# Optimization experiments

Measured on AMD Instinct MI355X. Metric: run time of the kernel, lower is better.

Reference implementation:

```python
import jax, jax.numpy as jnp
import numpy as np

N = 100000      # nodes
E = 3200000     # edges (before self loops)
F_IN = 5        # node_features
SH = 32         # spatial_hidden
H = 8           # heads
C = SH // H     # per-head dim = 4
TH = 64         # temporal_hidden
TC = TH // 3    # 21 (trend/seasonal lstm hidden)
TR = TH - 2 * TC  # 22 (residual mlp)
SEQ = 14
CV_THRESH = 1.5


def setup_inputs() -> dict:
    key = jax.random.key(0)
    cnt = [0]
    def nk():
        cnt[0] += 1
        return jax.random.fold_in(key, cnt[0])
    def nrm(shape, s=0.1):
        return jax.random.normal(nk(), shape, jnp.float32) * s
    inp = {}
    inp['x'] = nrm((N, F_IN), 1.0)
    inp['edge_index'] = jax.random.randint(nk(), (2, E), 0, N)
    inp['trend'] = nrm((1, SEQ), 1.0)
    inp['seasonal'] = nrm((1, SEQ), 1.0)
    inp['residual'] = nrm((1, SEQ), 1.0)
    inp['cv_values'] = jax.random.uniform(nk(), (1,), jnp.float32, 0.0, 3.0)
    inp['target_store_idx'] = 42
    # GAT layers: layer0 in=F_IN, layers 1,2 in=SH
    for i, din in enumerate([F_IN, SH, SH]):
        inp[f'gat_W{i}'] = nrm((din, SH), 1.0 / np.sqrt(din))
        inp[f'gat_as{i}'] = nrm((H, C))
        inp[f'gat_ad{i}'] = nrm((H, C))
        inp[f'gat_b{i}'] = jnp.zeros((SH,), jnp.float32)
    # two 2-layer LSTMs (input sizes 1 then TC), PyTorch gate order i,f,g,o
    for p in ('t', 's'):
        for l, din in enumerate([1, TC]):
            inp[f'{p}_Wih{l}'] = nrm((4 * TC, din), 1.0 / np.sqrt(TC))
            inp[f'{p}_Whh{l}'] = nrm((4 * TC, TC), 1.0 / np.sqrt(TC))
            inp[f'{p}_bih{l}'] = jnp.zeros((4 * TC,), jnp.float32)
            inp[f'{p}_bhh{l}'] = jnp.zeros((4 * TC,), jnp.float32)
    inp['res_W'] = nrm((1, TR), 1.0)
    inp['res_b'] = jnp.zeros((TR,), jnp.float32)
    FU = SH + TH  # 96
    inp['pg_W'] = nrm((FU + 1, FU), 1.0 / np.sqrt(FU))
    inp['pg_b'] = jnp.zeros((FU,), jnp.float32)
    inp['f1_W'] = nrm((FU, TH), 1.0 / np.sqrt(FU))
    inp['f1_b'] = jnp.zeros((TH,), jnp.float32)
    inp['ln_g'] = jnp.ones((TH,), jnp.float32)
    inp['ln_b'] = jnp.zeros((TH,), jnp.float32)
    inp['f2_W'] = nrm((TH, TH // 2), 1.0 / np.sqrt(TH))
    inp['f2_b'] = jnp.zeros((TH // 2,), jnp.float32)
    inp['f3_W'] = nrm((TH // 2, SEQ), 1.0 / np.sqrt(TH // 2))
    inp['f3_b'] = jnp.zeros((SEQ,), jnp.float32)
    return inp


def _gat(h_in, src, dst, W, a_s, a_d, b):
    # PyG GATConv: message src->dst, softmax over incoming edges per dst
    h = (h_in @ W).reshape(-1, H, C)            # [N,H,C]
    es = jnp.einsum('nhc,hc->nh', h, a_s)       # [N,H]
    ed = jnp.einsum('nhc,hc->nh', h, a_d)
    e = jax.nn.leaky_relu(es[src] + ed[dst], 0.2)  # [Etot,H]
    emax = jax.ops.segment_max(e, dst, num_segments=N)
    emax = jnp.where(jnp.isfinite(emax), emax, 0.0)
    a = jnp.exp(e - emax[dst])
    den = jax.ops.segment_sum(a, dst, num_segments=N)
    a = a / (den[dst] + 1e-16)
    out = jax.ops.segment_sum(h[src] * a[..., None], dst, num_segments=N)
    return out.reshape(-1, H * C) + b


def _lstm2(x, params):
    # x: [B,T,in]; params: list of (Wih[4h,in], Whh[4h,h], bih, bhh)
    seq = x
    for (Wih, Whh, bih, bhh) in params:
        B = seq.shape[0]
        hh = Whh.shape[1]
        def step(carry, xt):
            hprev, cprev = carry
            g = xt @ Wih.T + hprev @ Whh.T + bih + bhh
            i, f, gg, o = jnp.split(g, 4, axis=-1)
            c = jax.nn.sigmoid(f) * cprev + jax.nn.sigmoid(i) * jnp.tanh(gg)
            hn = jax.nn.sigmoid(o) * jnp.tanh(c)
            return (hn, c), hn
        init = (jnp.zeros((B, hh), seq.dtype), jnp.zeros((B, hh), seq.dtype))
        _, ys = jax.lax.scan(step, init, jnp.swapaxes(seq, 0, 1))
        seq = jnp.swapaxes(ys, 0, 1)
    return seq


def _forward(x, trend, seasonal, residual, cv_values,
             gat_params, lstm_t, lstm_s,
             res_W, res_b, pg_W, pg_b,
             f1_W, f1_b, ln_g, ln_b, f2_W, f2_b, f3_W, f3_b,
             edge_index, target_store_idx):
    loops = jnp.arange(N, dtype=edge_index.dtype)  # add_self_loops=True
    src = jnp.concatenate([edge_index[0], loops])
    dst = jnp.concatenate([edge_index[1], loops])
    h = x
    for (W, a_s, a_d, b) in gat_params:
        h = jax.nn.elu(_gat(h, src, dst, W, a_s, a_d, b))
    target_spatial = h[target_store_idx][None, :]          # [1,SH]
    trend_out = _lstm2(trend[..., None], lstm_t)[:, -1, :]      # [1,TC]
    seasonal_out = _lstm2(seasonal[..., None], lstm_s)[:, -1, :]
    res_out = jax.nn.relu(residual[..., None] @ res_W + res_b)[:, -1, :]  # [1,TR]
    temporal = jnp.concatenate([trend_out, seasonal_out, res_out], -1)    # [1,TH]
    combined = jnp.concatenate([target_spatial, temporal], -1)            # [1,96]
    gated_in = jnp.concatenate([combined, cv_values[:, None]], -1)        # [1,97]
    gate = jax.nn.sigmoid(gated_in @ pg_W + pg_b)
    gf = combined * gate
    h1 = gf @ f1_W + f1_b
    mu = h1.mean(-1, keepdims=True)
    var = h1.var(-1, keepdims=True)
    h1 = jax.nn.relu((h1 - mu) / jnp.sqrt(var + 1e-5) * ln_g + ln_b)
    h2 = jax.nn.relu(h1 @ f2_W + f2_b)
    return h2 @ f3_W + f3_b                                 # [1,SEQ]


def reference(x, edge_index, trend, seasonal, residual, cv_values, target_store_idx,
              gat_W0, gat_as0, gat_ad0, gat_b0,
              gat_W1, gat_as1, gat_ad1, gat_b1,
              gat_W2, gat_as2, gat_ad2, gat_b2,
              t_Wih0, t_Whh0, t_bih0, t_bhh0, t_Wih1, t_Whh1, t_bih1, t_bhh1,
              s_Wih0, s_Whh0, s_bih0, s_bhh0, s_Wih1, s_Whh1, s_bih1, s_bhh1,
              res_W, res_b, pg_W, pg_b,
              f1_W, f1_b, ln_g, ln_b, f2_W, f2_b, f3_W, f3_b):
    gat_params = [(gat_W0, gat_as0, gat_ad0, gat_b0),
                  (gat_W1, gat_as1, gat_ad1, gat_b1),
                  (gat_W2, gat_as2, gat_ad2, gat_b2)]
    lstm_t = [(t_Wih0, t_Whh0, t_bih0, t_bhh0), (t_Wih1, t_Whh1, t_bih1, t_bhh1)]
    lstm_s = [(s_Wih0, s_Whh0, s_bih0, s_bhh0), (s_Wih1, s_Whh1, s_bih1, s_bhh1)]
    return _forward(x, trend, seasonal, residual, cv_values,
                    gat_params, lstm_t, lstm_s,
                    res_W, res_b, pg_W, pg_b,
                    f1_W, f1_b, ln_g, ln_b, f2_W, f2_b, f3_W, f3_b,
                    edge_index, target_store_idx)
```

## Files before the change

kernel.cpp:

```cpp
#include <hip/hip_runtime.h>
#include <hip/hip_bf16.h>
#include <stdint.h>
#include <math.h>

#define NN   100000
#define EE   3200000
#define FIN  5
#define SHD  32
#define NH   8
#define TCH  21
#define TRH  22
#define SEQL 14

#define ECA   1024
#define ECL1  1024
#define ECL2  8192
#define RSTR  96

#define BCHK2 4096
#define NBC2  ((EE + BCHK2 - 1) / BCHK2)
#define NBW   ((NN + 31) / 32)
#define NBWP  3200

typedef __hip_bfloat16 bf16;
typedef __attribute__((ext_vector_type(2))) float f32x2;

__device__ __forceinline__ float b2f(bf16 v) { return __bfloat162float(v); }
__device__ __forceinline__ float sigm(float x) { return 1.f / (1.f + __expf(-x)); }
__device__ __forceinline__ float ldw(const void* p, int i, int f) {
    return f ? ((const float*)p)[i] : __bfloat162float(((const bf16*)p)[i]);
}
__device__ __forceinline__ float relu_nan(float v) {
    return (v == v) ? ((v > 0.f) ? v : 0.f) : v;
}
__device__ __forceinline__ unsigned short f2b(float v) {
    bf16 b = __float2bfloat16(v);
    return *reinterpret_cast<unsigned short*>(&b);
}
__device__ __forceinline__ float cvf(float v) { return v; }
__device__ __forceinline__ float cvf(bf16 v) { return __bfloat162float(v); }
__device__ __forceinline__ void cp(float* dst, const void* src, int n,
                                   int t0, int stride, int f) {
    if (f) {
        const float* s = (const float*)src;
        for (int i = t0; i < n; i += stride) dst[i] = s[i];
    } else {
        const bf16* s = (const bf16*)src;
        for (int i = t0; i < n; i += stride) dst[i] = b2f(s[i]);
    }
}

__global__ void PatternAwareSTGAT_94489281309_kernel(const unsigned int* xw, int* flag,
        const void* as0, const void* b0, const void* as1, const void* b1,
        const void* as2, const void* b2, float* prm) {
    int tid = threadIdx.x;
    int sane = 0;
    for (int i = 0; i < 64; i++) {
        unsigned int lo = xw[i] & 0xFFFFu;
        int e = (int)((lo >> 7) & 0xFF);
        if (e >= 110 && e <= 135) sane++;
    }
    int f = (sane >= 32) ? 0 : 1;
    if (tid == 0) flag[0] = f;
    const void* asp[3] = {as0, as1, as2};
    const void* bp[3]  = {b0, b1, b2};
    for (int l = 0; l < 3; l++)
        prm[l * 64 + tid] = (tid < 32) ? ldw(asp[l], tid, f) : ldw(bp[l], tid - 32, f);
}

__global__ __launch_bounds__(256) void k_scanA(
        const int* __restrict__ ei, const int* __restrict__ tgtp,
        int* __restrict__ eA, int* __restrict__ cA,
        unsigned* __restrict__ bm1, int* __restrict__ l1, int* __restrict__ c1,
        unsigned* __restrict__ bm2, int* __restrict__ l2, int* __restrict__ c2,
        int* __restrict__ l3, int* __restrict__ c3) {
    int tid = threadIdx.x;
    int tgtv = tgtp[0];
    if (blockIdx.x == 0 && tid == 0) {
        unsigned bit = 1u << (tgtv & 31);
        unsigned old = atomicOr(&bm1[tgtv >> 5], bit);
        if (!(old & bit)) { int p = atomicAdd(c1, 1); if (p < ECL1) l1[p] = tgtv; }
        old = atomicOr(&bm2[tgtv >> 5], bit);
        if (!(old & bit)) { int p = atomicAdd(c2, 1); if (p < ECL2) l2[p] = tgtv; }
        l3[0] = tgtv; c3[0] = 1;
    }
    int e0 = blockIdx.x * BCHK2 + tid * 16;
    if (e0 >= EE) return;
    const int4* dd4 = (const int4*)(ei + EE + e0);
    int4 a = dd4[0], b = dd4[1], c = dd4[2], d = dd4[3];
    int dv[16];
    dv[0]=a.x; dv[1]=a.y; dv[2]=a.z; dv[3]=a.w;
    dv[4]=b.x; dv[5]=b.y; dv[6]=b.z; dv[7]=b.w;
    dv[8]=c.x; dv[9]=c.y; dv[10]=c.z; dv[11]=c.w;
    dv[12]=d.x; dv[13]=d.y; dv[14]=d.z; dv[15]=d.w;
    unsigned mask = 0;
#pragma unroll
    for (int j = 0; j < 16; j++) if (dv[j] == tgtv) mask |= (1u << j);
    if (!mask) return;
#pragma unroll
    for (int j = 0; j < 16; j++) {
        if (mask & (1u << j)) {
            int s = ei[e0 + j];
            int p = atomicAdd(cA, 1);
            if (p < ECA) eA[p] = s;
            unsigned bit = 1u << (s & 31);
            unsigned old = atomicOr(&bm1[s >> 5], bit);
            if (!(old & bit)) { int q = atomicAdd(c1, 1); if (q < ECL1) l1[q] = s; }
            old = atomicOr(&bm2[s >> 5], bit);
            if (!(old & bit)) { int q = atomicAdd(c2, 1); if (q < ECL2) l2[q] = s; }
        }
    }
}

__global__ __launch_bounds__(256) void k_scanR(
        const int* __restrict__ ei, const unsigned* __restrict__ bm,
        int* __restrict__ fill, int* __restrict__ rows,
        unsigned* __restrict__ bmN, int* __restrict__ lN,
        int* __restrict__ cN, int capN) {
    __shared__ unsigned sbm[NBWP];
    int tid = threadIdx.x;
    {
        const uint4* b4 = (const uint4*)bm;
        uint4* s4 = (uint4*)sbm;
        uint4 t0 = b4[tid];
        uint4 t1 = b4[tid + 256];
        uint4 t2 = (tid + 512 < NBWP / 4) ? b4[tid + 512] : make_uint4(0,0,0,0);
        uint4 t3 = (tid + 768 < NBWP / 4) ? b4[tid + 768] : make_uint4(0,0,0,0);
        s4[tid] = t0;
        s4[tid + 256] = t1;
        if (tid + 512 < NBWP / 4) s4[tid + 512] = t2;
        if (tid + 768 < NBWP / 4) s4[tid + 768] = t3;
    }
    __syncthreads();
    int e0 = blockIdx.x * BCHK2 + tid * 16;
    if (e0 >= EE) return;
    const int4* dd4 = (const int4*)(ei + EE + e0);
    int4 a = dd4[0], b = dd4[1], c = dd4[2], d = dd4[3];
    int dv[16];
    dv[0]=a.x; dv[1]=a.y; dv[2]=a.z; dv[3]=a.w;
    dv[4]=b.x; dv[5]=b.y; dv[6]=b.z; dv[7]=b.w;
    dv[8]=c.x; dv[9]=c.y; dv[10]=c.z; dv[11]=c.w;
    dv[12]=d.x; dv[13]=d.y; dv[14]=d.z; dv[15]=d.w;
    unsigned mask = 0;
#pragma unroll
    for (int j = 0; j < 16; j++)
        if ((sbm[dv[j] >> 5] >> (dv[j] & 31)) & 1u) mask |= (1u << j);
    if (!mask) return;
#pragma unroll
    for (int j = 0; j < 16; j++) {
        if (mask & (1u << j)) {
            int dn = dv[j];
            int s = ei[e0 + j];
            int p = atomicAdd(&fill[dn], 1);
            if (p < RSTR) rows[(size_t)dn * RSTR + p] = s;
            if (bmN) {
                unsigned bit = 1u << (s & 31);
                unsigned old = atomicOr(&bmN[s >> 5], bit);
                if (!(old & bit)) {
                    int q = atomicAdd(cN, 1);
                    if (q < capN) lN[q] = s;
                }
            }
        }
    }
}

__global__ void k_transform0(const void* x, const void* W, const void* ad_,
                             const int* flag, unsigned short* hWb, float* ed) {
    __shared__ float sW[FIN * SHD];
    __shared__ float sad[SHD];
    int tid = threadIdx.x;
    int f = flag[0];
    cp(sW, W, FIN * SHD, tid, 256, f);
    if (tid >= 192 && tid < 192 + SHD) sad[tid - 192] = ldw(ad_, tid - 192, f);
    __syncthreads();
    int n = blockIdx.x * 256 + tid;
    if (n >= NN) return;
    float xr[FIN];
    if (f) {
        const float* xp = (const float*)x + (size_t)n * FIN;
        for (int k = 0; k < FIN; k++) xr[k] = xp[k];
    } else {
        const bf16* xp = (const bf16*)x + (size_t)n * FIN;
        for (int k = 0; k < FIN; k++) xr[k] = b2f(xp[k]);
    }
    float o[SHD];
    for (int j = 0; j < SHD; j++) o[j] = 0.f;
    for (int k = 0; k < FIN; k++) {
        float xv = xr[k];
        for (int j = 0; j < SHD; j++) o[j] += xv * sW[k * SHD + j];
    }
    ushort4* row = (ushort4*)(hWb + (size_t)n * SHD);
    for (int q = 0; q < 8; q++) {
        ushort4 v; v.x = f2b(o[q*4]); v.y = f2b(o[q*4+1]); v.z = f2b(o[q*4+2]); v.w = f2b(o[q*4+3]);
        row[q] = v;
    }
    for (int h = 0; h < NH; h++) {
        float e2 = 0.f;
        for (int c = 0; c < 4; c++) e2 += o[h * 4 + c] * sad[h * 4 + c];
        ed[(size_t)n * NH + h] = e2;
    }
}

__global__ void k_transform1(const int* __restrict__ list, const int* __restrict__ cntp,
                             int cap,
                             const float* x, const void* W, const void* ad_,
                             const int* flag, unsigned short* hWb, float* ed) {
    __shared__ float sW[SHD * SHD];
    __shared__ float sad[SHD];
    int tid = threadIdx.x;
    int f = flag[0];
    cp(sW, W, SHD * SHD, tid, 256, f);
    if (tid >= 192 && tid < 192 + SHD) sad[tid - 192] = ldw(ad_, tid - 192, f);
    __syncthreads();
    int cnt = cntp[0]; if (cnt > cap) cnt = cap;
    int ii = blockIdx.x * 256 + tid;
    if (ii >= cnt) return;
    int n = list[ii];
    float xr[SHD];
    const float4* xp4 = (const float4*)(x + (size_t)n * SHD);
#pragma unroll
    for (int q = 0; q < 8; q++) {
        float4 v = xp4[q];
        xr[q*4] = v.x; xr[q*4+1] = v.y; xr[q*4+2] = v.z; xr[q*4+3] = v.w;
    }
    float o[SHD];
    for (int j = 0; j < SHD; j++) o[j] = 0.f;
    for (int k = 0; k < SHD; k++) {
        float xv = xr[k];
        for (int j = 0; j < SHD; j++) o[j] += xv * sW[k * SHD + j];
    }
    ushort4* row = (ushort4*)(hWb + (size_t)n * SHD);
    for (int q = 0; q < 8; q++) {
        ushort4 v; v.x = f2b(o[q*4]); v.y = f2b(o[q*4+1]); v.z = f2b(o[q*4+2]); v.w = f2b(o[q*4+3]);
        row[q] = v;
    }
    for (int h = 0; h < NH; h++) {
        float e2 = 0.f;
        for (int c = 0; c < 4; c++) e2 += o[h * 4 + c] * sad[h * 4 + c];
        ed[(size_t)n * NH + h] = e2;
    }
}

__global__ void k_aggregate(const int* __restrict__ list, const int* __restrict__ cntp,
                            int cap,
                            const int* __restrict__ rdeg,
                            const int* __restrict__ csr,
                            const int* __restrict__ ovr, int ovrCap,
                            const unsigned short* __restrict__ hWb,
                            const float* __restrict__ ed,
                            const float* __restrict__ prm,
                            float* __restrict__ out) {
    int gid = blockIdx.x * 256 + threadIdx.x;
    int lane = threadIdx.x & 63;
    int cnt = cntp[0]; if (cnt > cap) cnt = cap;
    int idx = (gid >> 6) * 2 + (lane >> 5);
    if (idx >= cnt) return;
    int n = list[idx];
    int l32 = lane & 31;
    int h = l32 & 7, k = l32 >> 3;
    float4 asv = *(const float4*)(prm + h * 4);
    float ednh = ed[(size_t)n * NH + h];
    int base, deg;
    if (ovr) { base = 0; deg = ovr[0]; if (deg > ovrCap) deg = ovrCap; }
    else     { base = n * RSTR; deg = rdeg[n]; if (deg > RSTR) deg = RSTR; }
    float den = 0.f;
    f32x2 acc01 = {0.f, 0.f}, acc23 = {0.f, 0.f};
    int t = k;
    int s0 = -1, s1 = -1, s2 = -1, s3 = -1, s4 = -1, s5 = -1;
    if (t <= deg)      s0 = (t == 0) ? n : __builtin_nontemporal_load(csr + base + t - 1);
    if (t + 4 <= deg)  s1 = __builtin_nontemporal_load(csr + base + t + 3);
    if (t + 8 <= deg)  s2 = __builtin_nontemporal_load(csr + base + t + 7);
    if (t + 12 <= deg) s3 = __builtin_nontemporal_load(csr + base + t + 11);
    if (t + 16 <= deg) s4 = __builtin_nontemporal_load(csr + base + t + 15);
    if (t + 20 <= deg) s5 = __builtin_nontemporal_load(csr + base + t + 19);
    while (s0 >= 0) {
        uint2 hv0 = *(const uint2*)(hWb + (size_t)s0 * SHD + h * 4);
        bool b1 = (s1 >= 0), b2 = (s2 >= 0), b3 = (s3 >= 0), b4 = (s4 >= 0), b5 = (s5 >= 0);
        uint2 hv1, hv2, hv3, hv4, hv5;
        if (b1) hv1 = *(const uint2*)(hWb + (size_t)s1 * SHD + h * 4);
        if (b2) hv2 = *(const uint2*)(hWb + (size_t)s2 * SHD + h * 4);
        if (b3) hv3 = *(const uint2*)(hWb + (size_t)s3 * SHD + h * 4);
        if (b4) hv4 = *(const uint2*)(hWb + (size_t)s4 * SHD + h * 4);
        if (b5) hv5 = *(const uint2*)(hWb + (size_t)s5 * SHD + h * 4);
        int tn = t + 24;
        int p0 = -1, p1 = -1, p2 = -1, p3 = -1, p4 = -1, p5 = -1;
        if (tn <= deg)      p0 = __builtin_nontemporal_load(csr + base + tn - 1);
        if (tn + 4 <= deg)  p1 = __builtin_nontemporal_load(csr + base + tn + 3);
        if (tn + 8 <= deg)  p2 = __builtin_nontemporal_load(csr + base + tn + 7);
        if (tn + 12 <= deg) p3 = __builtin_nontemporal_load(csr + base + tn + 11);
        if (tn + 16 <= deg) p4 = __builtin_nontemporal_load(csr + base + tn + 15);
        if (tn + 20 <= deg) p5 = __builtin_nontemporal_load(csr + base + tn + 19);
        {
            f32x2 h01, h23;
            h01.x = __uint_as_float(hv0.x << 16);
            h01.y = __uint_as_float(hv0.x & 0xffff0000u);
            h23.x = __uint_as_float(hv0.y << 16);
            h23.y = __uint_as_float(hv0.y & 0xffff0000u);
            f32x2 d2 = h01 * (f32x2){asv.x, asv.y} + h23 * (f32x2){asv.z, asv.w};
            float e = d2.x + d2.y + ednh;
            e = fmaxf(e, 0.2f * e);
            float a = __expf(e);
            den += a;
            f32x2 av = {a, a};
            acc01 += av * h01;
            acc23 += av * h23;
        }
        if (b1) {
            f32x2 h01, h23;
            h01.x = __uint_as_float(hv1.x << 16);
            h01.y = __uint_as_float(hv1.x & 0xffff0000u);
            h23.x = __uint_as_float(hv1.y << 16);
            h23.y = __uint_as_float(hv1.y & 0xffff0000u);
            f32x2 d2 = h01 * (f32x2){asv.x, asv.y} + h23 * (f32x2){asv.z, asv.w};
            float e = d2.x + d2.y + ednh;
            e = fmaxf(e, 0.2f * e);
            float a = __expf(e);
            den += a;
            f32x2 av = {a, a};
            acc01 += av * h01;
            acc23 += av * h23;
        }
        if (b2) {
            f32x2 h01, h23;
            h01.x = __uint_as_float(hv2.x << 16);
            h01.y = __uint_as_float(hv2.x & 0xffff0000u);
            h23.x = __uint_as_float(hv2.y << 16);
            h23.y = __uint_as_float(hv2.y & 0xffff0000u);
            f32x2 d2 = h01 * (f32x2){asv.x, asv.y} + h23 * (f32x2){asv.z, asv.w};
            float e = d2.x + d2.y + ednh;
            e = fmaxf(e, 0.2f * e);
            float a = __expf(e);
            den += a;
            f32x2 av = {a, a};
            acc01 += av * h01;
            acc23 += av * h23;
        }
        if (b3) {
            f32x2 h01, h23;
            h01.x = __uint_as_float(hv3.x << 16);
            h01.y = __uint_as_float(hv3.x & 0xffff0000u);
            h23.x = __uint_as_float(hv3.y << 16);
            h23.y = __uint_as_float(hv3.y & 0xffff0000u);
            f32x2 d2 = h01 * (f32x2){asv.x, asv.y} + h23 * (f32x2){asv.z, asv.w};
            float e = d2.x + d2.y + ednh;
            e = fmaxf(e, 0.2f * e);
            float a = __expf(e);
            den += a;
            f32x2 av = {a, a};
            acc01 += av * h01;
            acc23 += av * h23;
        }
        if (b4) {
            f32x2 h01, h23;
            h01.x = __uint_as_float(hv4.x << 16);
            h01.y = __uint_as_float(hv4.x & 0xffff0000u);
            h23.x = __uint_as_float(hv4.y << 16);
            h23.y = __uint_as_float(hv4.y & 0xffff0000u);
            f32x2 d2 = h01 * (f32x2){asv.x, asv.y} + h23 * (f32x2){asv.z, asv.w};
            float e = d2.x + d2.y + ednh;
            e = fmaxf(e, 0.2f * e);
            float a = __expf(e);
            den += a;
            f32x2 av = {a, a};
            acc01 += av * h01;
            acc23 += av * h23;
        }
        if (b5) {
            f32x2 h01, h23;
            h01.x = __uint_as_float(hv5.x << 16);
            h01.y = __uint_as_float(hv5.x & 0xffff0000u);
            h23.x = __uint_as_float(hv5.y << 16);
            h23.y = __uint_as_float(hv5.y & 0xffff0000u);
            f32x2 d2 = h01 * (f32x2){asv.x, asv.y} + h23 * (f32x2){asv.z, asv.w};
            float e = d2.x + d2.y + ednh;
            e = fmaxf(e, 0.2f * e);
            float a = __expf(e);
            den += a;
            f32x2 av = {a, a};
            acc01 += av * h01;
            acc23 += av * h23;
        }
        s0 = p0; s1 = p1; s2 = p2; s3 = p3; s4 = p4; s5 = p5; t = tn;
    }
    for (int off = 16; off >= 8; off >>= 1) {
        den      += __shfl_down(den, off, 32);
        acc01.x  += __shfl_down(acc01.x, off, 32);
        acc01.y  += __shfl_down(acc01.y, off, 32);
        acc23.x  += __shfl_down(acc23.x, off, 32);
        acc23.y  += __shfl_down(acc23.y, off, 32);
    }
    if (k == 0) {
        float inv = 1.f / (den + 1e-16f);
        float4 bv = *(const float4*)(prm + 32 + h * 4);
        float v0 = acc01.x * inv + bv.x;
        float v1 = acc01.y * inv + bv.y;
        float v2 = acc23.x * inv + bv.z;
        float v3 = acc23.y * inv + bv.w;
        v0 = (v0 > 0.f) ? v0 : expm1f(v0);
        v1 = (v1 > 0.f) ? v1 : expm1f(v1);
        v2 = (v2 > 0.f) ? v2 : expm1f(v2);
        v3 = (v3 > 0.f) ? v3 : expm1f(v3);
        *(float4*)(out + (size_t)n * SHD + h * 4) = make_float4(v0, v1, v2, v3);
    }
}

template<typename T>
__device__ __forceinline__ void lstm_load_regs(
        const T* Wih0, const T* Whh0, const T* bih0, const T* bhh0,
        const T* Wih1, const T* Whh1, const T* bih1, const T* bhh1,
        const T* xin, int l, bool bl, float* xs,
        float& wa, float& ba, float& wb, float& bb, float& ba2, float& bb2,
        float* Wa, float* Wb, float* Ua, float* Va, float* Ub, float* Vb) {
#pragma unroll
    for (int t = 0; t < SEQL; t++) xs[t] = cvf(xin[t]);
    wa = cvf(Wih0[l]);
    ba = cvf(bih0[l]) + cvf(bhh0[l]);
    wb = bl ? cvf(Wih0[64 + l]) : 0.f;
    bb = bl ? (cvf(bih0[64 + l]) + cvf(bhh0[64 + l])) : 0.f;
    ba2 = cvf(bih1[l]) + cvf(bhh1[l]);
    bb2 = bl ? (cvf(bih1[64 + l]) + cvf(bhh1[64 + l])) : 0.f;
#pragma unroll
    for (int j = 0; j < 21; j++) {
        Wa[j] = cvf(Whh0[l * 21 + j]);
        Wb[j] = bl ? cvf(Whh0[(64 + l) * 21 + j]) : 0.f;
        Ua[j] = cvf(Wih1[l * 21 + j]);
        Va[j] = cvf(Whh1[l * 21 + j]);
        Ub[j] = bl ? cvf(Wih1[(64 + l) * 21 + j]) : 0.f;
        Vb[j] = bl ? cvf(Whh1[(64 + l) * 21 + j]) : 0.f;
    }
}

__device__ __forceinline__ void warm_sweep(const void* p, int nbytes, int t2) {
    const uint4* s = (const uint4*)p;
    int nv = nbytes >> 4;
    unsigned acc = 0;
    for (int i = t2; i < nv; i += 1024) {
        uint4 v0 = s[i];
        uint4 v1 = (i + 128 < nv) ? s[i + 128] : make_uint4(0,0,0,0);
        uint4 v2 = (i + 256 < nv) ? s[i + 256] : make_uint4(0,0,0,0);
        uint4 v3 = (i + 384 < nv) ? s[i + 384] : make_uint4(0,0,0,0);
        uint4 v4 = (i + 512 < nv) ? s[i + 512] : make_uint4(0,0,0,0);
        uint4 v5 = (i + 640 < nv) ? s[i + 640] : make_uint4(0,0,0,0);
        uint4 v6 = (i + 768 < nv) ? s[i + 768] : make_uint4(0,0,0,0);
        uint4 v7 = (i + 896 < nv) ? s[i + 896] : make_uint4(0,0,0,0);
        acc ^= v0.x ^ v1.x ^ v2.x ^ v3.x ^ v4.x ^ v5.x ^ v6.x ^ v7.x;
    }
    asm volatile("" :: "v"(acc));
}

template<typename T>
__device__ __forceinline__ float matvec_t(const T* W, const float* vin,
                                          float bias, int n, int col, int ncol) {
    float acc = bias;
    int k2 = 0;
    for (; k2 + 8 <= n; k2 += 8) {
        float w0 = cvf(W[(k2 + 0) * ncol + col]);
        float w1 = cvf(W[(k2 + 1) * ncol + col]);
        float w2 = cvf(W[(k2 + 2) * ncol + col]);
        float w3 = cvf(W[(k2 + 3) * ncol + col]);
        float w4 = cvf(W[(k2 + 4) * ncol + col]);
        float w5 = cvf(W[(k2 + 5) * ncol + col]);
        float w6 = cvf(W[(k2 + 6) * ncol + col]);
        float w7 = cvf(W[(k2 + 7) * ncol + col]);
        acc += vin[k2 + 0] * w0; acc += vin[k2 + 1] * w1;
        acc += vin[k2 + 2] * w2; acc += vin[k2 + 3] * w3;
        acc += vin[k2 + 4] * w4; acc += vin[k2 + 5] * w5;
        acc += vin[k2 + 6] * w6; acc += vin[k2 + 7] * w7;
    }
    for (; k2 < n; k2++) acc += vin[k2] * cvf(W[k2 * ncol + col]);
    return acc;
}
__device__ __forceinline__ float matvec(const void* W, const float* vin,
                                        float bias, int n, int col, int ncol, int f) {
    return f ? matvec_t<float>((const float*)W, vin, bias, n, col, ncol)
             : matvec_t<bf16>((const bf16*)W, vin, bias, n, col, ncol);
}

__global__ __launch_bounds__(256, 1)
void k_tail(const void* trend, const void* seasonal, const void* residual,
                       const void* cv, const int* tgtp,
                       const void* tWih0, const void* tWhh0, const void* tbih0, const void* tbhh0,
                       const void* tWih1, const void* tWhh1, const void* tbih1, const void* tbhh1,
                       const void* sWih0, const void* sWhh0, const void* sbih0, const void* sbhh0,
                       const void* sWih1, const void* sWhh1, const void* sbih1, const void* sbhh1,
                       const void* res_W, const void* res_b,
                       const void* pg_W, const void* pg_b,
                       const void* f1_W, const void* f1_b,
                       const void* ln_g, const void* ln_b,
                       const void* f2_W, const void* f2_b,
                       const void* f3_W, const void* f3_b,
                       const int* flag, const float* A, void* out) {
    __shared__ __align__(16) float SH1[2][24];
    __shared__ __align__(16) float SH2[2][24];
    __shared__ float comb[97];
    __shared__ float gf[96];
    __shared__ float h1v[64];
    __shared__ float h2s[32];
    __shared__ float sbias[336];
    __shared__ float stats[2];
    const int tid = threadIdx.x;
    const int f = flag[0];
    const int w = tid >> 6, l = tid & 63;

    if (tid < 96) {
        if (tid < 48) SH1[tid / 24][tid % 24] = 0.f;
        else { int u = tid - 48; SH2[u / 24][u % 24] = 0.f; }
    }
    __syncthreads();

    if (w < 2) {
        const void* Wih0 = w ? sWih0 : tWih0;
        const void* Whh0 = w ? sWhh0 : tWhh0;
        const void* bih0 = w ? sbih0 : tbih0;
        const void* bhh0 = w ? sbhh0 : tbhh0;
        const void* Wih1 = w ? sWih1 : tWih1;
        const void* Whh1 = w ? sWhh1 : tWhh1;
        const void* bih1 = w ? sbih1 : tbih1;
        const void* bhh1 = w ? sbhh1 : tbhh1;
        const void* xin  = w ? seasonal : trend;
        const bool bl = (l < 20);
        float xs[SEQL];
        float wa, ba, wb, bb, ba2, bb2;
        float Wa[21], Wb[21], Ua[21], Va[21], Ub[21], Vb[21];
        if (f) {
            lstm_load_regs<float>((const float*)Wih0, (const float*)Whh0,
                (const float*)bih0, (const float*)bhh0,
                (const float*)Wih1, (const float*)Whh1,
                (const float*)bih1, (const float*)bhh1,
                (const float*)xin, l, bl, xs, wa, ba, wb, bb, ba2, bb2,
                Wa, Wb, Ua, Va, Ub, Vb);
        } else {
            lstm_load_regs<bf16>((const bf16*)Wih0, (const bf16*)Whh0,
                (const bf16*)bih0, (const bf16*)bhh0,
                (const bf16*)Wih1, (const bf16*)Whh1,
                (const bf16*)bih1, (const bf16*)bhh1,
                (const bf16*)xin, l, bl, xs, wa, ba, wb, bb, ba2, bb2,
                Wa, Wb, Ua, Va, Ub, Vb);
        }
#pragma unroll
        for (int j = 0; j < 21; j++) {
            asm volatile("" : "+v"(Wa[j]), "+v"(Wb[j]));
            asm volatile("" : "+v"(Ua[j]), "+v"(Va[j]));
            asm volatile("" : "+v"(Ub[j]), "+v"(Vb[j]));
        }
#pragma unroll
        for (int t = 0; t < SEQL; t++) asm volatile("" : "+v"(xs[t]));
        asm volatile("" : "+v"(wa), "+v"(ba));
        asm volatile("" : "+v"(wb), "+v"(bb));
        asm volatile("" : "+v"(ba2), "+v"(bb2));

        float h1r = 0.f, c1v = 0.f, h2r = 0.f, c2v = 0.f;
#pragma unroll 1
        for (int t = 0; t < SEQL; t++) {
            float aa = ba + xs[t] * wa;
            float ab = bb + xs[t] * wb;
#pragma unroll
            for (int q = 0; q < 5; q++) {
                float4 v = *(const float4*)&SH1[w][q * 4];
                aa += v.x * Wa[q*4];   ab += v.x * Wb[q*4];
                aa += v.y * Wa[q*4+1]; ab += v.y * Wb[q*4+1];
                aa += v.z * Wa[q*4+2]; ab += v.z * Wb[q*4+2];
                aa += v.w * Wa[q*4+3]; ab += v.w * Wb[q*4+3];
            }
            { float v20 = SH1[w][20]; aa += v20 * Wa[20]; ab += v20 * Wb[20]; }
            float fj = __shfl(aa, 21 + l);
            float gj = __shfl(aa, 42 + l);
            float oa = __shfl(aa, 63);
            float ob = __shfl(ab, (l == 0) ? 0 : (l - 1));
            float oj = (l == 0) ? oa : ob;
            if (l < 21) {
                c1v = sigm(fj) * c1v + sigm(aa) * tanhf(gj);
                h1r = sigm(oj) * tanhf(c1v);
                SH1[w][l] = h1r;
            }
            __threadfence_block();
            float a2 = ba2, b2v = bb2;
#pragma unroll
            for (int q = 0; q < 5; q++) {
                float4 u = *(const float4*)&SH1[w][q * 4];
                float4 v = *(const float4*)&SH2[w][q * 4];
                a2  += u.x * Ua[q*4]   + v.x * Va[q*4];
                b2v += u.x * Ub[q*4]   + v.x * Vb[q*4];
                a2  += u.y * Ua[q*4+1] + v.y * Va[q*4+1];
                b2v += u.y * Ub[q*4+1] + v.y * Vb[q*4+1];
                a2  += u.z * Ua[q*4+2] + v.z * Va[q*4+2];
                b2v += u.z * Ub[q*4+2] + v.z * Vb[q*4+2];
                a2  += u.w * Ua[q*4+3] + v.w * Va[q*4+3];
                b2v += u.w * Ub[q*4+3] + v.w * Vb[q*4+3];
            }
            { float u20 = SH1[w][20], v20 = SH2[w][20];
              a2  += u20 * Ua[20] + v20 * Va[20];
              b2v += u20 * Ub[20] + v20 * Vb[20]; }
            float fj2 = __shfl(a2, 21 + l);
            float gj2 = __shfl(a2, 42 + l);
            float oa2 = __shfl(a2, 63);
            float ob2 = __shfl(b2v, (l == 0) ? 0 : (l - 1));
            float oj2 = (l == 0) ? oa2 : ob2;
            if (l < 21) {
                c2v = sigm(fj2) * c2v + sigm(a2) * tanhf(gj2);
                h2r = sigm(oj2) * tanhf(c2v);
                SH2[w][l] = h2r;
            }
            __threadfence_block();
        }
        if (l < 21) comb[(w == 0 ? 32 : 53) + l] = h2r;
    } else {
        int t2 = tid - 128;
        if (t2 < TRH)
            comb[74 + t2] = relu_nan(ldw(residual, SEQL - 1, f) * ldw(res_W, t2, f)
                                     + ldw(res_b, t2, f));
        if (t2 == TRH) comb[96] = ldw(cv, 0, f);
        if (t2 >= 32 && t2 < 64) {
            int tgt = tgtp[0];
            comb[t2 - 32] = A[(size_t)tgt * SHD + (t2 - 32)];
        }
        for (int i = t2; i < 336; i += 128) {
            float v;
            if (i < 96)       v = ldw(pg_b, i, f);
            else if (i < 160) v = ldw(f1_b, i - 96, f);
            else if (i < 192) v = ldw(f2_b, i - 160, f);
            else if (i < 206) v = ldw(f3_b, i - 192, f);
            else if (i < 208) v = 0.f;
            else if (i < 272) v = ldw(ln_g, i - 208, f);
            else              v = ldw(ln_b, i - 272, f);
            sbias[i] = v;
        }
        int esz = f ? 4 : 2;
        warm_sweep(pg_W, 9312 * esz, t2);
        warm_sweep(f1_W, 6144 * esz, t2);
        warm_sweep(f2_W, 2048 * esz, t2);
        warm_sweep(f3_W,  448 * esz, t2);
    }
    __syncthreads();

    if (tid < 96)
        gf[tid] = comb[tid] * sigm(matvec(pg_W, comb, sbias[tid], 97, tid, 96, f));
    __syncthreads();
    if (tid < 64)
        h1v[tid] = matvec(f1_W, gf, sbias[96 + tid], 96, tid, 64, f);
    __syncthreads();
    if (tid == 0) {
        float mu = 0.f;
        for (int j = 0; j < 64; j++) mu += h1v[j];
        mu /= 64.f;
        float var = 0.f;
        for (int j = 0; j < 64; j++) { float d = h1v[j] - mu; var += d * d; }
        var /= 64.f;
        stats[0] = mu; stats[1] = rsqrtf(var + 1e-5f);
    }
    __syncthreads();
    if (tid < 64)
        h1v[tid] = relu_nan((h1v[tid] - stats[0]) * stats[1] * sbias[208 + tid] + sbias[272 + tid]);
    __syncthreads();
    if (tid < 32)
        h2s[tid] = relu_nan(matvec(f2_W, h1v, sbias[160 + tid], 64, tid, 32, f));
    __syncthreads();
    if (tid < SEQL) {
        float acc = matvec(f3_W, h2s, sbias[192 + tid], 32, tid, 14, f);
        if (acc != acc) acc = 3333.0f;
        if (f) ((float*)out)[tid] = acc;
        else   ((bf16*)out)[tid] = __float2bfloat16(acc);
    }
}

static inline unsigned short h_f2bf(float f) {
    union { float f; unsigned u; } x; x.f = f;
    return (unsigned short)(x.u >> 16);
}
static unsigned short g_diag[SEQL];

extern "C" void kernel_launch(void* const* d_in, const int* in_sizes, int n_in,
                              void* d_out, int out_size, void* d_ws, size_t ws_size,
                              hipStream_t stream) {
    const int* ei  = (const int*)d_in[1];
    const int* tgt = (const int*)d_in[6];

    const size_t HWB  = sizeof(unsigned short) * (size_t)NN * SHD;
    const size_t EDB  = sizeof(float) * (size_t)NN * NH;
    const size_t AB   = sizeof(float) * (size_t)NN * SHD;
    const size_t ZER  = sizeof(int) * (size_t)(16 + 2 * NBWP + 2 * NN);
    const size_t ROWB = sizeof(int) * (size_t)NN * RSTR;
    const size_t LSTB = sizeof(int) * (size_t)(ECA + ECL1 + 8 + ECL2);
    const size_t NEED = 256 + 1024 + ZER + LSTB + 2 * ROWB + 512 + HWB + EDB + AB;
    if (ws_size < NEED) {
        for (int i = 0; i < SEQL; i++) g_diag[i] = h_f2bf(7777.0f);
        hipMemcpyAsync(d_out, g_diag, SEQL * sizeof(unsigned short),
                       hipMemcpyHostToDevice, stream);
        return;
    }

    char* p = (char*)d_ws;
    int*   flag = (int*)p;   p += 256;
    float* prm  = (float*)p; p += 1024;
    int* cnts  = (int*)p; p += sizeof(int) * 16;
    unsigned* bm1 = (unsigned*)p; p += sizeof(int) * NBWP;
    unsigned* bm2 = (unsigned*)p; p += sizeof(int) * NBWP;
    int* fillB = (int*)p; p += sizeof(int) * NN;
    int* fillC = (int*)p; p += sizeof(int) * NN;
    int* eA   = (int*)p; p += sizeof(int) * ECA;
    int* l1   = (int*)p; p += sizeof(int) * ECL1;
    int* l3   = (int*)p; p += sizeof(int) * 8;
    int* l2   = (int*)p; p += sizeof(int) * ECL2;
    int* rowsB = (int*)p; p += ROWB;
    int* rowsC = (int*)p; p += ROWB;
    p = (char*)(((uintptr_t)p + 255) & ~(uintptr_t)255);
    unsigned short* hWb = (unsigned short*)p; p += HWB;
    float* ed = (float*)p; p += EDB;
    float* A  = (float*)p; p += AB;
    int* cA = cnts; int* c1 = cnts + 1; int* c2 = cnts + 2; int* c3 = cnts + 3;

    dim3 b256(256);
    dim3 gN((NN + 255) / 256);
    dim3 gScan(NBC2);

    PatternAwareSTGAT_94489281309_kernel<<<dim3(1), dim3(64), 0, stream>>>(
        (const unsigned int*)d_in[0], flag,
        d_in[8], d_in[10], d_in[12], d_in[14], d_in[16], d_in[18], prm);

    hipMemsetAsync(cnts, 0, ZER, stream);

    k_scanA<<<gScan, b256, 0, stream>>>(ei, tgt, eA, cA,
                                        bm1, l1, c1, bm2, l2, c2, l3, c3);
    k_scanR<<<gScan, b256, 0, stream>>>(ei, bm1, fillB, rowsB,
                                        bm2, l2, c2, ECL2);
    k_scanR<<<gScan, b256, 0, stream>>>(ei, bm2, fillC, rowsC,
                                        (unsigned*)nullptr, (int*)nullptr,
                                        (int*)nullptr, 0);

    k_transform0<<<gN, b256, 0, stream>>>(d_in[0], d_in[7], d_in[9], flag, hWb, ed);
    k_aggregate<<<dim3(ECL2 * 32 / 256), b256, 0, stream>>>(l2, c2, ECL2,
        fillC, rowsC, (const int*)nullptr, 0, hWb, ed, prm, A);
    k_transform1<<<dim3(ECL2 / 256), b256, 0, stream>>>(l2, c2, ECL2,
        A, d_in[11], d_in[13], flag, hWb, ed);
    k_aggregate<<<dim3(ECL1 * 32 / 256), b256, 0, stream>>>(l1, c1, ECL1,
        fillB, rowsB, (const int*)nullptr, 0, hWb, ed, prm + 64, A);
    k_transform1<<<dim3((ECL1 + 255) / 256), b256, 0, stream>>>(l1, c1, ECL1,
        A, d_in[15], d_in[17], flag, hWb, ed);
    k_aggregate<<<dim3(1), b256, 0, stream>>>(l3, c3, 8,
        (const int*)nullptr, eA, cA, ECA, hWb, ed, prm + 128, A);

    k_tail<<<dim3(1), b256, 0, stream>>>(
        d_in[2], d_in[3], d_in[4], d_in[5], tgt,
        d_in[19], d_in[20], d_in[21], d_in[22],
        d_in[23], d_in[24], d_in[25], d_in[26],
        d_in[27], d_in[28], d_in[29], d_in[30],
        d_in[31], d_in[32], d_in[33], d_in[34],
        d_in[35], d_in[36],
        d_in[37], d_in[38],
        d_in[39], d_in[40],
        d_in[41], d_in[42],
        d_in[43], d_in[44],
        d_in[45], d_in[46],
        flag, A, d_out);
}
```

Before: 255.6 us.

## Fuse final-layer target aggregation into tail kernel and drop separate edge list

The third GAT layer's aggregation for the single target node now runs inside the tail kernel, in one spare warp, reading the existing rowsB CSR rows instead of a dedicated eA edge list. This removes one kernel launch, the A round-trip for the target row, and the per-match atomics into eA and cA inside the scan. The sanity check in the setup kernel now uses a wavefront ballot instead of a serial 64-element loop. The tradeoff is that the fused aggregation runs in a single warp and sits on the tail kernel's critical path, and the target's degree is capped at RSTR where the old list allowed up to ECA.

```diff
diff --git a/kernel.cpp b/kernel.cpp
--- a/kernel.cpp
+++ b/kernel.cpp
@@ -12,7 +12,6 @@
 #define TRH  22
 #define SEQL 14
 
-#define ECA   1024
 #define ECL1  1024
 #define ECL2  8192
 #define RSTR  96
@@ -54,12 +53,10 @@
         const void* as0, const void* b0, const void* as1, const void* b1,
         const void* as2, const void* b2, float* prm) {
     int tid = threadIdx.x;
-    int sane = 0;
-    for (int i = 0; i < 64; i++) {
-        unsigned int lo = xw[i] & 0xFFFFu;
-        int e = (int)((lo >> 7) & 0xFF);
-        if (e >= 110 && e <= 135) sane++;
-    }
+    unsigned int lo = xw[tid] & 0xFFFFu;
+    int e = (int)((lo >> 7) & 0xFF);
+    bool ok = (e >= 110 && e <= 135);
+    int sane = __popcll(__ballot(ok));
     int f = (sane >= 32) ? 0 : 1;
     if (tid == 0) flag[0] = f;
     const void* asp[3] = {as0, as1, as2};
@@ -70,10 +67,8 @@
 
 __global__ __launch_bounds__(256) void k_scanA(
         const int* __restrict__ ei, const int* __restrict__ tgtp,
-        int* __restrict__ eA, int* __restrict__ cA,
         unsigned* __restrict__ bm1, int* __restrict__ l1, int* __restrict__ c1,
-        unsigned* __restrict__ bm2, int* __restrict__ l2, int* __restrict__ c2,
-        int* __restrict__ l3, int* __restrict__ c3) {
+        unsigned* __restrict__ bm2, int* __restrict__ l2, int* __restrict__ c2) {
     int tid = threadIdx.x;
     int tgtv = tgtp[0];
     if (blockIdx.x == 0 && tid == 0) {
@@ -82,7 +77,6 @@
         if (!(old & bit)) { int p = atomicAdd(c1, 1); if (p < ECL1) l1[p] = tgtv; }
         old = atomicOr(&bm2[tgtv >> 5], bit);
         if (!(old & bit)) { int p = atomicAdd(c2, 1); if (p < ECL2) l2[p] = tgtv; }
-        l3[0] = tgtv; c3[0] = 1;
     }
     int e0 = blockIdx.x * BCHK2 + tid * 16;
     if (e0 >= EE) return;
@@ -101,8 +95,6 @@
     for (int j = 0; j < 16; j++) {
         if (mask & (1u << j)) {
             int s = ei[e0 + j];
-            int p = atomicAdd(cA, 1);
-            if (p < ECA) eA[p] = s;
             unsigned bit = 1u << (s & 31);
             unsigned old = atomicOr(&bm1[s >> 5], bit);
             if (!(old & bit)) { int q = atomicAdd(c1, 1); if (q < ECL1) l1[q] = s; }
@@ -246,7 +238,6 @@
                             int cap,
                             const int* __restrict__ rdeg,
                             const int* __restrict__ csr,
-                            const int* __restrict__ ovr, int ovrCap,
                             const unsigned short* __restrict__ hWb,
                             const float* __restrict__ ed,
                             const float* __restrict__ prm,
@@ -261,9 +252,8 @@
     int h = l32 & 7, k = l32 >> 3;
     float4 asv = *(const float4*)(prm + h * 4);
     float ednh = ed[(size_t)n * NH + h];
-    int base, deg;
-    if (ovr) { base = 0; deg = ovr[0]; if (deg > ovrCap) deg = ovrCap; }
-    else     { base = n * RSTR; deg = rdeg[n]; if (deg > RSTR) deg = RSTR; }
+    int base = n * RSTR;
+    int deg = rdeg[n]; if (deg > RSTR) deg = RSTR;
     float den = 0.f;
     f32x2 acc01 = {0.f, 0.f}, acc23 = {0.f, 0.f};
     int t = k;
@@ -490,10 +480,15 @@
                        const void* ln_g, const void* ln_b,
                        const void* f2_W, const void* f2_b,
                        const void* f3_W, const void* f3_b,
-                       const int* flag, const float* A, void* out) {
+                       const int* flag,
+                       const int* __restrict__ rowsB, const int* __restrict__ fillB,
+                       const unsigned short* __restrict__ hWb,
+                       const float* __restrict__ ed,
+                       const float* __restrict__ prm3,
+                       void* out) {
     __shared__ __align__(16) float SH1[2][24];
     __shared__ __align__(16) float SH2[2][24];
-    __shared__ float comb[97];
+    __shared__ __align__(16) float comb[100];
     __shared__ float gf[96];
     __shared__ float h1v[64];
     __shared__ float h2s[32];
@@ -611,10 +606,6 @@
             comb[74 + t2] = relu_nan(ldw(residual, SEQL - 1, f) * ldw(res_W, t2, f)
                                      + ldw(res_b, t2, f));
         if (t2 == TRH) comb[96] = ldw(cv, 0, f);
-        if (t2 >= 32 && t2 < 64) {
-            int tgt = tgtp[0];
-            comb[t2 - 32] = A[(size_t)tgt * SHD + (t2 - 32)];
-        }
         for (int i = t2; i < 336; i += 128) {
             float v;
             if (i < 96)       v = ldw(pg_b, i, f);
@@ -631,6 +622,155 @@
         warm_sweep(f1_W, 6144 * esz, t2);
         warm_sweep(f2_W, 2048 * esz, t2);
         warm_sweep(f3_W,  448 * esz, t2);
+
+        if (w == 2 && l < 32) {
+            int tgt = tgtp[0];
+            int h = l & 7, k = l >> 3;
+            float4 asv = *(const float4*)(prm3 + h * 4);
+            float ednh = ed[(size_t)tgt * NH + h];
+            int base = tgt * RSTR;
+            int deg = fillB[tgt]; if (deg > RSTR) deg = RSTR;
+            float den = 0.f;
+            f32x2 acc01 = {0.f, 0.f}, acc23 = {0.f, 0.f};
+            int t = k;
+            int s0 = -1, s1 = -1, s2 = -1, s3 = -1, s4 = -1, s5 = -1;
+            if (t <= deg)      s0 = (t == 0) ? tgt : rowsB[base + t - 1];
+            if (t + 4 <= deg)  s1 = rowsB[base + t + 3];
+            if (t + 8 <= deg)  s2 = rowsB[base + t + 7];
+            if (t + 12 <= deg) s3 = rowsB[base + t + 11];
+            if (t + 16 <= deg) s4 = rowsB[base + t + 15];
+            if (t + 20 <= deg) s5 = rowsB[base + t + 19];
+            while (s0 >= 0) {
+                uint2 hv0 = *(const uint2*)(hWb + (size_t)s0 * SHD + h * 4);
+                bool b1 = (s1 >= 0), b2 = (s2 >= 0), b3 = (s3 >= 0),
+                     b4 = (s4 >= 0), b5 = (s5 >= 0);
+                uint2 hv1, hv2, hv3, hv4, hv5;
+                if (b1) hv1 = *(const uint2*)(hWb + (size_t)s1 * SHD + h * 4);
+                if (b2) hv2 = *(const uint2*)(hWb + (size_t)s2 * SHD + h * 4);
+                if (b3) hv3 = *(const uint2*)(hWb + (size_t)s3 * SHD + h * 4);
+                if (b4) hv4 = *(const uint2*)(hWb + (size_t)s4 * SHD + h * 4);
+                if (b5) hv5 = *(const uint2*)(hWb + (size_t)s5 * SHD + h * 4);
+                int tn = t + 24;
+                int p0 = -1, p1 = -1, p2 = -1, p3 = -1, p4 = -1, p5 = -1;
+                if (tn <= deg)      p0 = rowsB[base + tn - 1];
+                if (tn + 4 <= deg)  p1 = rowsB[base + tn + 3];
+                if (tn + 8 <= deg)  p2 = rowsB[base + tn + 7];
+                if (tn + 12 <= deg) p3 = rowsB[base + tn + 11];
+                if (tn + 16 <= deg) p4 = rowsB[base + tn + 15];
+                if (tn + 20 <= deg) p5 = rowsB[base + tn + 19];
+                {
+                    f32x2 h01, h23;
+                    h01.x = __uint_as_float(hv0.x << 16);
+                    h01.y = __uint_as_float(hv0.x & 0xffff0000u);
+                    h23.x = __uint_as_float(hv0.y << 16);
+                    h23.y = __uint_as_float(hv0.y & 0xffff0000u);
+                    f32x2 d2 = h01 * (f32x2){asv.x, asv.y} + h23 * (f32x2){asv.z, asv.w};
+                    float e = d2.x + d2.y + ednh;
+                    e = fmaxf(e, 0.2f * e);
+                    float a = __expf(e);
+                    den += a;
+                    f32x2 av = {a, a};
+                    acc01 += av * h01;
+                    acc23 += av * h23;
+                }
+                if (b1) {
+                    f32x2 h01, h23;
+                    h01.x = __uint_as_float(hv1.x << 16);
+                    h01.y = __uint_as_float(hv1.x & 0xffff0000u);
+                    h23.x = __uint_as_float(hv1.y << 16);
+                    h23.y = __uint_as_float(hv1.y & 0xffff0000u);
+                    f32x2 d2 = h01 * (f32x2){asv.x, asv.y} + h23 * (f32x2){asv.z, asv.w};
+                    float e = d2.x + d2.y + ednh;
+                    e = fmaxf(e, 0.2f * e);
+                    float a = __expf(e);
+                    den += a;
+                    f32x2 av = {a, a};
+                    acc01 += av * h01;
+                    acc23 += av * h23;
+                }
+                if (b2) {
+                    f32x2 h01, h23;
+                    h01.x = __uint_as_float(hv2.x << 16);
+                    h01.y = __uint_as_float(hv2.x & 0xffff0000u);
+                    h23.x = __uint_as_float(hv2.y << 16);
+                    h23.y = __uint_as_float(hv2.y & 0xffff0000u);
+                    f32x2 d2 = h01 * (f32x2){asv.x, asv.y} + h23 * (f32x2){asv.z, asv.w};
+                    float e = d2.x + d2.y + ednh;
+                    e = fmaxf(e, 0.2f * e);
+                    float a = __expf(e);
+                    den += a;
+                    f32x2 av = {a, a};
+                    acc01 += av * h01;
+                    acc23 += av * h23;
+                }
+                if (b3) {
+                    f32x2 h01, h23;
+                    h01.x = __uint_as_float(hv3.x << 16);
+                    h01.y = __uint_as_float(hv3.x & 0xffff0000u);
+                    h23.x = __uint_as_float(hv3.y << 16);
+                    h23.y = __uint_as_float(hv3.y & 0xffff0000u);
+                    f32x2 d2 = h01 * (f32x2){asv.x, asv.y} + h23 * (f32x2){asv.z, asv.w};
+                    float e = d2.x + d2.y + ednh;
+                    e = fmaxf(e, 0.2f * e);
+                    float a = __expf(e);
+                    den += a;
+                    f32x2 av = {a, a};
+                    acc01 += av * h01;
+                    acc23 += av * h23;
+                }
+                if (b4) {
+                    f32x2 h01, h23;
+                    h01.x = __uint_as_float(hv4.x << 16);
+                    h01.y = __uint_as_float(hv4.x & 0xffff0000u);
+                    h23.x = __uint_as_float(hv4.y << 16);
+                    h23.y = __uint_as_float(hv4.y & 0xffff0000u);
+                    f32x2 d2 = h01 * (f32x2){asv.x, asv.y} + h23 * (f32x2){asv.z, asv.w};
+                    float e = d2.x + d2.y + ednh;
+                    e = fmaxf(e, 0.2f * e);
+                    float a = __expf(e);
+                    den += a;
+                    f32x2 av = {a, a};
+                    acc01 += av * h01;
+                    acc23 += av * h23;
+                }
+                if (b5) {
+                    f32x2 h01, h23;
+                    h01.x = __uint_as_float(hv5.x << 16);
+                    h01.y = __uint_as_float(hv5.x & 0xffff0000u);
+                    h23.x = __uint_as_float(hv5.y << 16);
+                    h23.y = __uint_as_float(hv5.y & 0xffff0000u);
+                    f32x2 d2 = h01 * (f32x2){asv.x, asv.y} + h23 * (f32x2){asv.z, asv.w};
+                    float e = d2.x + d2.y + ednh;
+                    e = fmaxf(e, 0.2f * e);
+                    float a = __expf(e);
+                    den += a;
+                    f32x2 av = {a, a};
+                    acc01 += av * h01;
+                    acc23 += av * h23;
+                }
+                s0 = p0; s1 = p1; s2 = p2; s3 = p3; s4 = p4; s5 = p5; t = tn;
+            }
+            for (int off = 16; off >= 8; off >>= 1) {
+                den      += __shfl_down(den, off, 32);
+                acc01.x  += __shfl_down(acc01.x, off, 32);
+                acc01.y  += __shfl_down(acc01.y, off, 32);
+                acc23.x  += __shfl_down(acc23.x, off, 32);
+                acc23.y  += __shfl_down(acc23.y, off, 32);
+            }
+            if (k == 0) {
+                float inv = 1.f / (den + 1e-16f);
+                float4 bv = *(const float4*)(prm3 + 32 + h * 4);
+                float v0 = acc01.x * inv + bv.x;
+                float v1 = acc01.y * inv + bv.y;
+                float v2 = acc23.x * inv + bv.z;
+                float v3 = acc23.y * inv + bv.w;
+                v0 = (v0 > 0.f) ? v0 : expm1f(v0);
+                v1 = (v1 > 0.f) ? v1 : expm1f(v1);
+                v2 = (v2 > 0.f) ? v2 : expm1f(v2);
+                v3 = (v3 > 0.f) ? v3 : expm1f(v3);
+                *(float4*)(&comb[h * 4]) = make_float4(v0, v1, v2, v3);
+            }
+        }
     }
     __syncthreads();
 
@@ -681,7 +821,7 @@
     const size_t AB   = sizeof(float) * (size_t)NN * SHD;
     const size_t ZER  = sizeof(int) * (size_t)(16 + 2 * NBWP + 2 * NN);
     const size_t ROWB = sizeof(int) * (size_t)NN * RSTR;
-    const size_t LSTB = sizeof(int) * (size_t)(ECA + ECL1 + 8 + ECL2);
+    const size_t LSTB = sizeof(int) * (size_t)(ECL1 + ECL2);
     const size_t NEED = 256 + 1024 + ZER + LSTB + 2 * ROWB + 512 + HWB + EDB + AB;
     if (ws_size < NEED) {
         for (int i = 0; i < SEQL; i++) g_diag[i] = h_f2bf(7777.0f);
@@ -698,9 +838,7 @@
     unsigned* bm2 = (unsigned*)p; p += sizeof(int) * NBWP;
     int* fillB = (int*)p; p += sizeof(int) * NN;
     int* fillC = (int*)p; p += sizeof(int) * NN;
-    int* eA   = (int*)p; p += sizeof(int) * ECA;
     int* l1   = (int*)p; p += sizeof(int) * ECL1;
-    int* l3   = (int*)p; p += sizeof(int) * 8;
     int* l2   = (int*)p; p += sizeof(int) * ECL2;
     int* rowsB = (int*)p; p += ROWB;
     int* rowsC = (int*)p; p += ROWB;
@@ -708,7 +846,7 @@
     unsigned short* hWb = (unsigned short*)p; p += HWB;
     float* ed = (float*)p; p += EDB;
     float* A  = (float*)p; p += AB;
-    int* cA = cnts; int* c1 = cnts + 1; int* c2 = cnts + 2; int* c3 = cnts + 3;
+    int* c1 = cnts; int* c2 = cnts + 1;
 
     dim3 b256(256);
     dim3 gN((NN + 255) / 256);
@@ -720,8 +858,7 @@
 
     hipMemsetAsync(cnts, 0, ZER, stream);
 
-    k_scanA<<<gScan, b256, 0, stream>>>(ei, tgt, eA, cA,
-                                        bm1, l1, c1, bm2, l2, c2, l3, c3);
+    k_scanA<<<gScan, b256, 0, stream>>>(ei, tgt, bm1, l1, c1, bm2, l2, c2);
     k_scanR<<<gScan, b256, 0, stream>>>(ei, bm1, fillB, rowsB,
                                         bm2, l2, c2, ECL2);
     k_scanR<<<gScan, b256, 0, stream>>>(ei, bm2, fillC, rowsC,
@@ -730,15 +867,13 @@
 
     k_transform0<<<gN, b256, 0, stream>>>(d_in[0], d_in[7], d_in[9], flag, hWb, ed);
     k_aggregate<<<dim3(ECL2 * 32 / 256), b256, 0, stream>>>(l2, c2, ECL2,
-        fillC, rowsC, (const int*)nullptr, 0, hWb, ed, prm, A);
+        fillC, rowsC, hWb, ed, prm, A);
     k_transform1<<<dim3(ECL2 / 256), b256, 0, stream>>>(l2, c2, ECL2,
         A, d_in[11], d_in[13], flag, hWb, ed);
     k_aggregate<<<dim3(ECL1 * 32 / 256), b256, 0, stream>>>(l1, c1, ECL1,
-        fillB, rowsB, (const int*)nullptr, 0, hWb, ed, prm + 64, A);
+        fillB, rowsB, hWb, ed, prm + 64, A);
     k_transform1<<<dim3((ECL1 + 255) / 256), b256, 0, stream>>>(l1, c1, ECL1,
         A, d_in[15], d_in[17], flag, hWb, ed);
-    k_aggregate<<<dim3(1), b256, 0, stream>>>(l3, c3, 8,
-        (const int*)nullptr, eA, cA, ECA, hWb, ed, prm + 128, A);
 
     k_tail<<<dim3(1), b256, 0, stream>>>(
         d_in[2], d_in[3], d_in[4], d_in[5], tgt,
@@ -752,5 +887,5 @@
         d_in[41], d_in[42],
         d_in[43], d_in[44],
         d_in[45], d_in[46],
-        flag, A, d_out);
-}
+        flag, rowsB, fillB, hWb, ed, prm + 128, d_out);
+}
```

After: 246.0 us. -3.7%, faster.
